# Kernel tuning notes

Measured on AMD Instinct MI355X. Metric: run time of the kernel, lower is better.

The kernel has to match this reference:

```python
import jax, jax.numpy as jnp
import numpy as np
import math

B, L, D, H = 2, 2048, 1024, 16
DH = D // H
TAU = 1.0
EPS_LN = 1e-12


def neural_sort(scores, tau=TAU):
    # scores: (B, n) -> soft permutation P_hat: (B, n, n)
    s = scores[..., None]                                   # (B,n,1)
    A = jnp.abs(s - jnp.swapaxes(s, 1, 2))                  # (B,n,n) pairwise |s_i - s_j|
    Bsum = jnp.sum(A, axis=-1, keepdims=True)               # row sums == A @ ones(n,n) columns
    n = scores.shape[-1]
    scaling = (n + 1 - 2 * (jnp.arange(n) + 1)).astype(scores.dtype)  # (n,)
    C = s * scaling[None, None, :]                          # (B,n,n)
    P_max = jnp.swapaxes(C - Bsum, 1, 2)
    return jax.nn.softmax(P_max / tau, axis=-1)


def euler_transform(v, delta, b_euler, log_scale, is_query):
    # v: (B,L,D); soft-sort channels, polar decompose, rotate, recompose
    Bv, Lv, Dv = v.shape
    scores = v.mean(axis=1)                                 # (B,D)
    P = neural_sort(scores)                                 # (B,D,D)
    v_sorted = jnp.einsum('bij,blj->bli', P, v)             # permute channel dim
    r, p = v_sorted[..., ::2], v_sorted[..., 1::2]          # (B,L,D/2)
    lam = jnp.sqrt(r * r + p * p + 1e-6)
    lam_d = jax.lax.stop_gradient(lam)
    theta = jnp.arctan2(p / lam_d, r / lam_d)
    theta = theta * delta
    if is_query:
        theta = theta + b_euler
    lam = lam * jnp.exp(jnp.clip(log_scale, -5.0, 5.0))
    out = jnp.stack([lam * jnp.cos(theta), lam * jnp.sin(theta)], axis=-1)
    return out.reshape(Bv, Lv, Dv)


def layer_norm(x, gamma, beta, eps=EPS_LN):
    mu = x.mean(axis=-1, keepdims=True)
    var = ((x - mu) ** 2).mean(axis=-1, keepdims=True)
    return (x - mu) / jnp.sqrt(var + eps) * gamma + beta


def forward(input_tensor, Wq, bq, Wk, bk, Wv, bv, Wd, bd, gamma, beta, delta, b_euler, log_scale):
    q = input_tensor @ Wq.T + bq
    k = input_tensor @ Wk.T + bk
    v = input_tensor @ Wv.T + bv
    q = euler_transform(q, delta, b_euler, log_scale, is_query=True)
    k = euler_transform(k, delta, b_euler, log_scale, is_query=False)
    def heads(x):
        return x.reshape(B, L, H, DH).transpose(0, 2, 1, 3)  # (B,H,L,DH)
    qh, kh, vh = heads(q), heads(k), heads(v)
    scores = jnp.einsum('bhqd,bhkd->bhqk', qh, kh) / math.sqrt(DH)
    probs = jax.nn.softmax(scores, axis=-1)                 # dropout off (eval)
    ctx = jnp.einsum('bhqk,bhkd->bhqd', probs, vh)
    ctx = ctx.transpose(0, 2, 1, 3).reshape(B, L, D)
    hidden = ctx @ Wd.T + bd
    return layer_norm(hidden + input_tensor, gamma, beta)


def setup_inputs() -> dict:
    key = jax.random.key(0)
    ks = jax.random.split(key, 16)
    s = 1.0 / math.sqrt(D)
    return {
        'input_tensor': jax.random.normal(ks[0], (B, L, D), jnp.float32),
        'Wq': jax.random.normal(ks[1], (D, D), jnp.float32) * s,
        'bq': jnp.zeros((D,), jnp.float32),
        'Wk': jax.random.normal(ks[2], (D, D), jnp.float32) * s,
        'bk': jnp.zeros((D,), jnp.float32),
        'Wv': jax.random.normal(ks[3], (D, D), jnp.float32) * s,
        'bv': jnp.zeros((D,), jnp.float32),
        'Wd': jax.random.normal(ks[4], (D, D), jnp.float32) * s,
        'bd': jnp.zeros((D,), jnp.float32),
        'gamma': jnp.ones((D,), jnp.float32),
        'beta': jnp.zeros((D,), jnp.float32),
        'delta': jnp.full((1, 1, D // 2), 0.1, jnp.float32),
        'b_euler': jnp.zeros((1, 1, D // 2), jnp.float32),
        'log_scale': jnp.zeros((1, 1, D // 2), jnp.float32),
    }


def reference(input_tensor, Wq, bq, Wk, bk, Wv, bv, Wd, bd, gamma, beta, delta, b_euler, log_scale):
    return forward(input_tensor, Wq, bq, Wk, bk, Wv, bv, Wd, bd, gamma, beta, delta, b_euler, log_scale)
```

## Files before the change

### kernel.cpp

```cpp
#include <hip/hip_runtime.h>


typedef unsigned short bf16_t;
typedef short frag_ab __attribute__((ext_vector_type(8)));
typedef float frag_cd __attribute__((ext_vector_type(4)));

#define BB 2
#define LL 2048
#define DD 1024
#define HH 16
#define DH 64

#define QSCALE 0.18033688f
#define EOFF  -17.3123404907f

__device__ __forceinline__ float b2f(bf16_t u) {
  union { unsigned int i; float f; } c; c.i = ((unsigned int)u) << 16; return c.f;
}
__device__ __forceinline__ bf16_t f2b(float f) {
  union { float f; unsigned int i; } c; c.f = f;
  unsigned int r = c.i + 0x7fffu + ((c.i >> 16) & 1u);
  return (bf16_t)(r >> 16);
}
__device__ __forceinline__ unsigned int fbits(float f) {
  union { float f; unsigned int i; } c; c.f = f; return c.i;
}
__device__ __forceinline__ float waveMax(float v) {
#pragma unroll
  for (int m = 32; m > 0; m >>= 1) v = fmaxf(v, __shfl_xor(v, m));
  return v;
}
__device__ __forceinline__ float waveSum(float v) {
#pragma unroll
  for (int m = 32; m > 0; m >>= 1) v += __shfl_xor(v, m);
  return v;
}

__device__ __forceinline__ void gll16(const bf16_t* g, bf16_t* l) {
  __builtin_amdgcn_global_load_lds(
      (const __attribute__((address_space(1))) void*)g,
      (__attribute__((address_space(3))) void*)l, 16, 0, 0);
}

__global__ __launch_bounds__(256) void prep_cast(const float* __restrict__ X,
                                                 const float* __restrict__ Wv,
                                                 const float* __restrict__ Wd,
                                                 bf16_t* __restrict__ Xb,
                                                 bf16_t* __restrict__ Wvb,
                                                 bf16_t* __restrict__ Wdb,
                                                 float* __restrict__ xmean) {
  const int bid = blockIdx.x;
  if (bid == 6144) {
    if (threadIdx.x < 256)
      for (int i = threadIdx.x; i < BB * DD; i += 256) xmean[i] = 0.f;
    return;
  }
  const float* in;
  bf16_t* out;
  int i;
  if (bid < 4096)      { in = X;  out = Xb;  i = bid * 256 + threadIdx.x; }
  else if (bid < 5120) { in = Wv; out = Wvb; i = (bid - 4096) * 256 + threadIdx.x; }
  else                 { in = Wd; out = Wdb; i = (bid - 5120) * 256 + threadIdx.x; }
  float4 v = ((const float4*)in)[i];
  ushort4 o;
  o.x = f2b(v.x); o.y = f2b(v.y); o.z = f2b(v.z); o.w = f2b(v.w);
  ((ushort4*)out)[i] = o;
}

__global__ __launch_bounds__(256) void cast_transpose_w(const float* __restrict__ Wq,
                                                        const float* __restrict__ Wk,
                                                        bf16_t* __restrict__ WqT,
                                                        bf16_t* __restrict__ WkT) {
  const float* W = blockIdx.z ? Wk : Wq;
  bf16_t* WT = blockIdx.z ? WkT : WqT;
  __shared__ bf16_t T[64][72];
  const int i0 = blockIdx.x * 64, m0 = blockIdx.y * 64;
  const int tid = threadIdx.x;
#pragma unroll
  for (int it = 0; it < 4; ++it) {
    const int idx = tid + it * 256;
    const int r = idx >> 4, c4 = (idx & 15) * 4;
    float4 v = *(const float4*)&W[(size_t)(i0 + r) * DD + m0 + c4];
    T[c4 + 0][r] = f2b(v.x);
    T[c4 + 1][r] = f2b(v.y);
    T[c4 + 2][r] = f2b(v.z);
    T[c4 + 3][r] = f2b(v.w);
  }
  __syncthreads();
#pragma unroll
  for (int it = 0; it < 2; ++it) {
    const int idx = tid + it * 256;
    const int r = idx >> 3, seg = idx & 7;
    *(uint4*)&WT[(size_t)(m0 + r) * DD + i0 + seg * 8] = *(const uint4*)&T[r][seg * 8];
  }
}

struct GemmB { const bf16_t* A; const bf16_t* Bm; const float* bias; float* Cf; bf16_t* Cb; };
struct GemmArgs { GemmB gb[6]; };

__global__ __launch_bounds__(256) void gemm128(GemmArgs ga, int M, int N, int K) {
  const GemmB g = ga.gb[blockIdx.z];
  const int bm = blockIdx.y * 128, bn = blockIdx.x * 128;
  __shared__ bf16_t As[128][32];
  __shared__ bf16_t Bs[128][32];
  bf16_t* As_f = &As[0][0];
  bf16_t* Bs_f = &Bs[0][0];
  const int tid = threadIdx.x;
  const int lane = tid & 63, w = tid >> 6;
  const int quad = lane >> 4, l16 = lane & 15;
  const int wm = (w >> 1) * 64, wn = (w & 1) * 64;
  const int wbase = w << 9;

  frag_cd acc[4][4];
#pragma unroll
  for (int i = 0; i < 4; ++i)
#pragma unroll
    for (int j = 0; j < 4; ++j)
#pragma unroll
      for (int r = 0; r < 4; ++r) acc[i][j][r] = 0.f;

  const int r0 = tid >> 2, s0 = (tid & 3) * 8;
  const int r1 = (tid + 256) >> 2, s1 = ((tid + 256) & 3) * 8;
  const size_t aoff0 = (size_t)(bm + r0) * K + s0;
  const size_t aoff1 = (size_t)(bm + r1) * K + s1;
  const size_t boff0 = (size_t)(bn + r0) * K + s0;
  const size_t boff1 = (size_t)(bn + r1) * K + s1;

  for (int k0 = 0; k0 < K; k0 += 32) {
    __syncthreads();
    gll16(g.A + aoff0 + k0, As_f + wbase);
    gll16(g.A + aoff1 + k0, As_f + 2048 + wbase);
    gll16(g.Bm + boff0 + k0, Bs_f + wbase);
    gll16(g.Bm + boff1 + k0, Bs_f + 2048 + wbase);
    __syncthreads();
    frag_ab af[4], bfr[4];
#pragma unroll
    for (int i = 0; i < 4; ++i) {
      af[i]  = *(const frag_ab*)&As[wm + i * 16 + l16][quad * 8];
      bfr[i] = *(const frag_ab*)&Bs[wn + i * 16 + l16][quad * 8];
    }
#pragma unroll
    for (int i = 0; i < 4; ++i)
#pragma unroll
      for (int j = 0; j < 4; ++j)
        acc[i][j] = __builtin_amdgcn_mfma_f32_16x16x32_bf16(af[i], bfr[j], acc[i][j], 0, 0, 0);
  }

#pragma unroll
  for (int i = 0; i < 4; ++i) {
#pragma unroll
    for (int r = 0; r < 4; ++r) {
      const int row = bm + wm + i * 16 + quad * 4 + r;
#pragma unroll
      for (int j = 0; j < 4; ++j) {
        const int col = bn + wn + j * 16 + l16;
        float v = acc[i][j][r];
        if (g.bias) v += g.bias[col];
        if (g.Cf) g.Cf[(size_t)row * N + col] = v;
        if (g.Cb) g.Cb[(size_t)row * N + col] = f2b(v);
      }
    }
  }
}

__global__ __launch_bounds__(256) void gemm64x64(GemmArgs ga, int M, int N, int K) {
  const GemmB g = ga.gb[blockIdx.z];
  const int bm = blockIdx.y * 64, bn = blockIdx.x * 64;
  __shared__ bf16_t As[64][32];
  __shared__ bf16_t Bs[64][32];
  bf16_t* As_f = &As[0][0];
  bf16_t* Bs_f = &Bs[0][0];
  const int tid = threadIdx.x;
  const int lane = tid & 63, w = tid >> 6;
  const int quad = lane >> 4, l16 = lane & 15;
  const int wm = (w >> 1) * 32, wn = (w & 1) * 32;
  const int wbase = w << 9;

  frag_cd acc[2][2];
#pragma unroll
  for (int i = 0; i < 2; ++i)
#pragma unroll
    for (int j = 0; j < 2; ++j)
#pragma unroll
      for (int r = 0; r < 4; ++r) acc[i][j][r] = 0.f;

  const int r0 = tid >> 2, s0 = (tid & 3) * 8;
  const size_t aoff0 = (size_t)(bm + r0) * K + s0;
  const size_t boff0 = (size_t)(bn + r0) * K + s0;

  for (int k0 = 0; k0 < K; k0 += 32) {
    __syncthreads();
    gll16(g.A + aoff0 + k0, As_f + wbase);
    gll16(g.Bm + boff0 + k0, Bs_f + wbase);
    __syncthreads();
    frag_ab af[2], bfr[2];
#pragma unroll
    for (int i = 0; i < 2; ++i) {
      af[i]  = *(const frag_ab*)&As[wm + i * 16 + l16][quad * 8];
      bfr[i] = *(const frag_ab*)&Bs[wn + i * 16 + l16][quad * 8];
    }
#pragma unroll
    for (int i = 0; i < 2; ++i)
#pragma unroll
      for (int j = 0; j < 2; ++j)
        acc[i][j] = __builtin_amdgcn_mfma_f32_16x16x32_bf16(af[i], bfr[j], acc[i][j], 0, 0, 0);
  }

#pragma unroll
  for (int i = 0; i < 2; ++i) {
#pragma unroll
    for (int r = 0; r < 4; ++r) {
      const int row = bm + wm + i * 16 + quad * 4 + r;
#pragma unroll
      for (int j = 0; j < 2; ++j) {
        const int col = bn + wn + j * 16 + l16;
        float v = acc[i][j][r];
        if (g.bias) v += g.bias[col];
        if (g.Cf) g.Cf[(size_t)row * N + col] = v;
        if (g.Cb) g.Cb[(size_t)row * N + col] = f2b(v);
      }
    }
  }
}

__global__ __launch_bounds__(256) void xmean_kernel(const float* __restrict__ X,
                                                    float* __restrict__ xmean) {
  const int d = blockIdx.x * 256 + threadIdx.x;
  const int b = blockIdx.z;
  const int l0 = blockIdx.y * 64;
  float s = 0.f;
  for (int l = l0; l < l0 + 64; ++l)
    s += X[((size_t)b * LL + l) * DD + d];
  atomicAdd(&xmean[b * DD + d], s * (1.f / (float)LL));
}

__global__ __launch_bounds__(256) void scores_gemm(const float* __restrict__ xmean,
                                                   const float* __restrict__ Wq,
                                                   const float* __restrict__ bq,
                                                   const float* __restrict__ Wk,
                                                   const float* __restrict__ bk,
                                                   float* __restrict__ scores) {
  const int w = threadIdx.x >> 6, lane = threadIdx.x & 63;
  const int idx = blockIdx.x * 4 + w;
  const int t = idx >> 11, b = (idx >> 10) & 1, i = idx & 1023;
  const float* W = t ? Wk : Wq;
  const float* bias = t ? bk : bq;
  const float* xm = xmean + b * DD;
  float sum = 0.f;
#pragma unroll
  for (int k = 0; k < 4; ++k) {
    float4 wv = *(const float4*)&W[(size_t)i * DD + k * 256 + lane * 4];
    float4 xv = *(const float4*)&xm[k * 256 + lane * 4];
    sum += wv.x * xv.x + wv.y * xv.y + wv.z * xv.z + wv.w * xv.w;
  }
  sum = waveSum(sum);
  if (lane == 0) scores[idx] = sum + bias[i];
}

__global__ __launch_bounds__(256) void bsum_kernel(const float* __restrict__ scores,
                                                   float* __restrict__ bsum) {
  __shared__ float sc[DD];
  const int z = blockIdx.x, jb = blockIdx.y, tid = threadIdx.x;
#pragma unroll
  for (int s = 0; s < 4; ++s) sc[tid + s * 256] = scores[z * DD + tid + s * 256];
  __syncthreads();
  const int j = jb * 256 + tid;
  const float si = sc[j];
  float s = 0.f;
  for (int m = 0; m < DD; m += 4) {
    float4 v = *(const float4*)&sc[m];
    s += fabsf(si - v.x) + fabsf(si - v.y) + fabsf(si - v.z) + fabsf(si - v.w);
  }
  bsum[z * DD + j] = s;
}

__global__ __launch_bounds__(256) void p_kernel(const float* __restrict__ scores,
                                                const float* __restrict__ bsum,
                                                const float* __restrict__ bq,
                                                const float* __restrict__ bk,
                                                bf16_t* __restrict__ Pq,
                                                bf16_t* __restrict__ Pk,
                                                float* __restrict__ bias4) {
  const int i = blockIdx.x;
  const int z = blockIdx.y;
  const int t = z >> 1, b = z & 1;
  const float* sc = scores + z * DD;
  const float* bs = bsum + z * DD;
  const float* bias = t ? bk : bq;
  const float scal = 1023.f - 2.f * (float)i;
  const int tid = threadIdx.x;
  __shared__ float redA[4], redB[4], redC[4];

  float lg[4], bb[4];
  float mx = -1e30f;
#pragma unroll
  for (int s = 0; s < 4; ++s) {
    const int j = tid + s * 256;
    lg[s] = sc[j] * scal - bs[j];
    bb[s] = bias[j];
    mx = fmaxf(mx, lg[s]);
  }
  mx = waveMax(mx);
  if ((tid & 63) == 0) redA[tid >> 6] = mx;
  __syncthreads();
  const float M = fmaxf(fmaxf(redA[0], redA[1]), fmaxf(redA[2], redA[3]));
  float sum = 0.f, dot = 0.f;
#pragma unroll
  for (int s = 0; s < 4; ++s) {
    lg[s] = __expf(lg[s] - M);
    sum += lg[s];
    dot += lg[s] * bb[s];
  }
  sum = waveSum(sum); dot = waveSum(dot);
  if ((tid & 63) == 0) { redB[tid >> 6] = sum; redC[tid >> 6] = dot; }
  __syncthreads();
  const float inv = 1.f / (redB[0] + redB[1] + redB[2] + redB[3]);
  bf16_t* P = (t ? Pk : Pq) + ((size_t)b << 20) + (size_t)i * DD;
#pragma unroll
  for (int s = 0; s < 4; ++s) P[tid + s * 256] = f2b(lg[s] * inv);
  if (tid == 0)
    bias4[t * 2048 + b * 1024 + i] = (redC[0] + redC[1] + redC[2] + redC[3]) * inv;
}

__global__ __launch_bounds__(256) void euler_transv(bf16_t* __restrict__ qs,
                                                    bf16_t* __restrict__ ks,
                                                    const float* __restrict__ delta,
                                                    const float* __restrict__ beul,
                                                    const float* __restrict__ lsc,
                                                    const bf16_t* __restrict__ vb,
                                                    bf16_t* __restrict__ vbT) {
  __shared__ bf16_t T[64][72];
  const int bid = blockIdx.x;
  const int tid = threadIdx.x;
  if (bid < 16384) {
    const int isq = (bid < 8192);
    unsigned int* buf = (unsigned int*)(isq ? qs : ks);
    const int idx = (isq ? bid : bid - 8192) * 256 + tid;
    const int c = idx & 511;
    const size_t n = idx >> 9;
    const unsigned int u = buf[n * 512 + c];
    const float r = b2f((bf16_t)(u & 0xffffu));
    const float p = b2f((bf16_t)(u >> 16));
    float lam = sqrtf(r * r + p * p + 1e-6f);
    float th = atan2f(p, r) * delta[c];
    if (isq) th += beul[c];
    lam *= __expf(fminf(fmaxf(lsc[c], -5.f), 5.f));
    if (isq) lam *= QSCALE;
    float sn, cs;
    __sincosf(th, &sn, &cs);
    buf[n * 512 + c] = ((unsigned int)f2b(lam * sn) << 16) | (unsigned int)f2b(lam * cs);
    return;
  }
  const int tb = bid - 16384;
  const int l0 = (tb & 31) * 64, d0 = ((tb >> 5) & 15) * 64, b = tb >> 9;
  for (int i = tid; i < 512; i += 256) {
    const int r = i >> 3, seg = i & 7;
    uint4 v = *(const uint4*)&vb[((size_t)b * LL + l0 + r) * DD + d0 + seg * 8];
    const bf16_t* vs = (const bf16_t*)&v;
#pragma unroll
    for (int j = 0; j < 8; ++j) T[seg * 8 + j][r] = vs[j];
  }
  __syncthreads();
  for (int i = tid; i < 512; i += 256) {
    const int r = i >> 3, seg = i & 7;
    *(uint4*)&vbT[((size_t)b * DD + d0 + r) * LL + l0 + seg * 8] =
        *(const uint4*)&T[r][seg * 8];
  }
}

__global__ __launch_bounds__(256) void attn_kernel(const bf16_t* __restrict__ Q,
                                                   const bf16_t* __restrict__ Kt,
                                                   const bf16_t* __restrict__ VT,
                                                   bf16_t* __restrict__ O) {
  const int bid = blockIdx.x;
  const int g = (bid & 7) + 8 * (bid >> 8);
  const int qt = (bid >> 3) & 31;
  const int b = g >> 4, h = g & 15;
  const int q0 = qt * 64;
  const int tid = threadIdx.x, w = tid >> 6, lane = tid & 63;
  const int quad = lane >> 4, l16 = lane & 15;
  __shared__ bf16_t Ks[64][72], Vs[80][72], Ps[64][72], Qs[64][72];
  const size_t base = ((size_t)b * LL) * DD + (size_t)h * DH;
  const size_t vtb = (size_t)(b * DD + h * DH) * LL;

  for (int i = tid; i < 16 * 72; i += 256) {
    const int r = i / 72;
    Vs[64 + r][i % 72] = (r == 0) ? (bf16_t)0x3F80 : (bf16_t)0;
  }
  for (int i = tid; i < 512; i += 256) {
    const int r = i >> 3, seg = i & 7;
    *(uint4*)&Qs[r][seg * 8] = *(const uint4*)&Q[base + (size_t)(q0 + r) * DD + seg * 8];
  }
  __syncthreads();
  frag_ab bq0 = *(const frag_ab*)&Qs[w * 16 + l16][quad * 8];
  frag_ab bq1 = *(const frag_ab*)&Qs[w * 16 + l16][32 + quad * 8];

  frag_cd o_[4], l5;
#pragma unroll
  for (int n = 0; n < 4; ++n)
#pragma unroll
    for (int r = 0; r < 4; ++r) o_[n][r] = 0.f;
#pragma unroll
  for (int r = 0; r < 4; ++r) l5[r] = 0.f;

  for (int kt = 0; kt < LL / 64; ++kt) {
    __syncthreads();
    for (int i = tid; i < 512; i += 256) {
      const int r = i >> 3, seg = i & 7;
      *(uint4*)&Ks[r][seg * 8] = *(const uint4*)&Kt[base + (size_t)(kt * 64 + r) * DD + seg * 8];
      *(uint4*)&Vs[r][seg * 8] = *(const uint4*)&VT[vtb + (size_t)r * LL + kt * 64 + seg * 8];
    }
    __syncthreads();

#pragma unroll
    for (int n = 0; n < 4; ++n) {
      frag_ab ak0 = *(const frag_ab*)&Ks[n * 16 + l16][quad * 8];
      frag_ab ak1 = *(const frag_ab*)&Ks[n * 16 + l16][32 + quad * 8];
      frag_cd z; z[0] = z[1] = z[2] = z[3] = EOFF;
      z = __builtin_amdgcn_mfma_f32_16x16x32_bf16(ak0, bq0, z, 0, 0, 0);
      z = __builtin_amdgcn_mfma_f32_16x16x32_bf16(ak1, bq1, z, 0, 0, 0);
      float p0 = __builtin_amdgcn_exp2f(z[0]);
      float p1 = __builtin_amdgcn_exp2f(z[1]);
      float p2 = __builtin_amdgcn_exp2f(z[2]);
      float p3 = __builtin_amdgcn_exp2f(z[3]);
      unsigned int u01 = __builtin_amdgcn_perm(fbits(p1), fbits(p0), 0x07060302u);
      unsigned int u23 = __builtin_amdgcn_perm(fbits(p3), fbits(p2), 0x07060302u);
      uint2 pk; pk.x = u01; pk.y = u23;
      *(uint2*)&Ps[w * 16 + l16][n * 16 + quad * 4] = pk;
    }

    frag_ab ap0 = *(const frag_ab*)&Ps[w * 16 + l16][quad * 8];
    frag_ab ap1 = *(const frag_ab*)&Ps[w * 16 + l16][32 + quad * 8];
#pragma unroll
    for (int n = 0; n < 4; ++n) {
      frag_ab bv0 = *(const frag_ab*)&Vs[n * 16 + l16][quad * 8];
      frag_ab bv1 = *(const frag_ab*)&Vs[n * 16 + l16][32 + quad * 8];
      o_[n] = __builtin_amdgcn_mfma_f32_16x16x32_bf16(ap0, bv0, o_[n], 0, 0, 0);
      o_[n] = __builtin_amdgcn_mfma_f32_16x16x32_bf16(ap1, bv1, o_[n], 0, 0, 0);
    }
    frag_ab bo0 = *(const frag_ab*)&Vs[64 + l16][quad * 8];
    frag_ab bo1 = *(const frag_ab*)&Vs[64 + l16][32 + quad * 8];
    l5 = __builtin_amdgcn_mfma_f32_16x16x32_bf16(ap0, bo0, l5, 0, 0, 0);
    l5 = __builtin_amdgcn_mfma_f32_16x16x32_bf16(ap1, bo1, l5, 0, 0, 0);
  }

  float lfin[4];
#pragma unroll
  for (int r = 0; r < 4; ++r) lfin[r] = 1.f / __shfl(l5[r], quad << 4);

#pragma unroll
  for (int n = 0; n < 4; ++n)
#pragma unroll
    for (int r = 0; r < 4; ++r) {
      const float v = o_[n][r] * lfin[r];
      O[base + (size_t)(q0 + w * 16 + quad * 4 + r) * DD + n * 16 + l16] = f2b(v);
    }
}

__global__ __launch_bounds__(256) void ln_kernel(const bf16_t* __restrict__ hidden,
                                                 const float* __restrict__ x0,
                                                 const float* __restrict__ gamma,
                                                 const float* __restrict__ beta,
                                                 float* __restrict__ out) {
  const int row = blockIdx.x;
  const int tid = threadIdx.x;
  __shared__ float red1[4], red2[4];
  float v[4];
  float s1 = 0.f, s2 = 0.f;
#pragma unroll
  for (int s = 0; s < 4; ++s) {
    const int c = tid + s * 256;
    const float x = b2f(hidden[(size_t)row * DD + c]) + x0[(size_t)row * DD + c];
    v[s] = x; s1 += x; s2 += x * x;
  }
  s1 = waveSum(s1); s2 = waveSum(s2);
  if ((tid & 63) == 0) { red1[tid >> 6] = s1; red2[tid >> 6] = s2; }
  __syncthreads();
  const float t1 = red1[0] + red1[1] + red1[2] + red1[3];
  const float t2 = red2[0] + red2[1] + red2[2] + red2[3];
  const float mu = t1 * (1.f / DD);
  const float var = t2 * (1.f / DD) - mu * mu;
  const float inv = rsqrtf(var + 1e-12f);
#pragma unroll
  for (int s = 0; s < 4; ++s) {
    const int c = tid + s * 256;
    out[(size_t)row * DD + c] = (v[s] - mu) * inv * gamma[c] + beta[c];
  }
}

extern "C" void kernel_launch(void* const* d_in, const int* in_sizes, int n_in,
                              void* d_out, int out_size, void* d_ws, size_t ws_size,
                              hipStream_t stream) {
  const float* X    = (const float*)d_in[0];
  const float* Wq   = (const float*)d_in[1];
  const float* bq   = (const float*)d_in[2];
  const float* Wk   = (const float*)d_in[3];
  const float* bk   = (const float*)d_in[4];
  const float* Wv   = (const float*)d_in[5];
  const float* bv   = (const float*)d_in[6];
  const float* Wd   = (const float*)d_in[7];
  const float* bd   = (const float*)d_in[8];
  const float* gam  = (const float*)d_in[9];
  const float* bet  = (const float*)d_in[10];
  const float* delt = (const float*)d_in[11];
  const float* beul = (const float*)d_in[12];
  const float* lsc  = (const float*)d_in[13];
  float* out = (float*)d_out;

  char* w = (char*)d_ws;
  const size_t MB = 1024ull * 1024ull;
  bf16_t* Xb  = (bf16_t*)(w + 0 * MB);
  bf16_t* Wvb = (bf16_t*)(w + 8 * MB);
  bf16_t* Wdb = (bf16_t*)(w + 10 * MB);
  bf16_t* WqT = (bf16_t*)(w + 12 * MB);
  bf16_t* WkT = (bf16_t*)(w + 14 * MB);
  bf16_t* Pq  = (bf16_t*)(w + 16 * MB);
  bf16_t* Pk  = (bf16_t*)(w + 20 * MB);
  bf16_t* Wp  = (bf16_t*)(w + 24 * MB);
  bf16_t* vb  = (bf16_t*)(w + 32 * MB);
  bf16_t* qs  = (bf16_t*)(w + 40 * MB);
  bf16_t* ks  = (bf16_t*)(w + 48 * MB);
  bf16_t* vbT = (bf16_t*)(w + 56 * MB);
  bf16_t* ctx = (bf16_t*)(w + 64 * MB);
  bf16_t* hid = (bf16_t*)(w + 24 * MB);
  float*  xmean  = (float*)(w + 72 * MB);
  float*  scores = (float*)(w + 72 * MB + 16384);
  float*  bsum   = (float*)(w + 72 * MB + 32768);
  float*  bias4  = (float*)(w + 72 * MB + 49152);

  const size_t WSZ = (size_t)DD * DD;

  prep_cast<<<dim3(6145), 256, 0, stream>>>(X, Wv, Wd, Xb, Wvb, Wdb, xmean);
  cast_transpose_w<<<dim3(16, 16, 2), 256, 0, stream>>>(Wq, Wk, WqT, WkT);

  xmean_kernel<<<dim3(4, 32, 2), 256, 0, stream>>>(X, xmean);
  scores_gemm<<<dim3(1024), 256, 0, stream>>>(xmean, Wq, bq, Wk, bk, scores);

  bsum_kernel<<<dim3(4, 4), 256, 0, stream>>>(scores, bsum);
  p_kernel<<<dim3(1024, 4), 256, 0, stream>>>(scores, bsum, bq, bk, Pq, Pk, bias4);

  GemmArgs gw = {};
  gw.gb[0] = {Pq,       WqT, nullptr, nullptr, Wp};
  gw.gb[1] = {Pq + WSZ, WqT, nullptr, nullptr, Wp + WSZ};
  gw.gb[2] = {Pk,       WkT, nullptr, nullptr, Wp + 2 * WSZ};
  gw.gb[3] = {Pk + WSZ, WkT, nullptr, nullptr, Wp + 3 * WSZ};
  gemm64x64<<<dim3(16, 16, 4), 256, 0, stream>>>(gw, DD, DD, DD);

  const size_t XHALF = (size_t)LL * DD;
  GemmArgs gs = {};
  gs.gb[0] = {Xb,         Wp,           bias4,        nullptr, qs};
  gs.gb[1] = {Xb + XHALF, Wp + WSZ,     bias4 + 1024, nullptr, qs + XHALF};
  gs.gb[2] = {Xb,         Wp + 2 * WSZ, bias4 + 2048, nullptr, ks};
  gs.gb[3] = {Xb + XHALF, Wp + 3 * WSZ, bias4 + 3072, nullptr, ks + XHALF};
  gs.gb[4] = {Xb,         Wvb,          bv,           nullptr, vb};
  gs.gb[5] = {Xb + XHALF, Wvb,          bv,           nullptr, vb + XHALF};
  gemm128<<<dim3(8, 16, 6), 256, 0, stream>>>(gs, LL, DD, DD);

  euler_transv<<<dim3(17408), 256, 0, stream>>>(qs, ks, delt, beul, lsc, vb, vbT);

  attn_kernel<<<dim3(1024), 256, 0, stream>>>(qs, ks, vbT, ctx);

  GemmArgs g4 = {};
  g4.gb[0] = {ctx, Wdb, bd, nullptr, hid};
  gemm64x64<<<dim3(16, 64, 1), 256, 0, stream>>>(g4, BB * LL, DD, DD);

  ln_kernel<<<dim3(BB * LL), 256, 0, stream>>>(hid, X, gam, bet, out);
}
```

Measured before the change: 310.7 us.

## Restructure attention kernel with double-buffered async LDS loads and swizzled tiles

Rewrites the attention kernel to use 128-thread blocks where each wave handles 32 query rows. K/V tiles are double-buffered and loaded with direct global-to-LDS loads under explicit vmcnt waits, so the next tile's load overlaps compute. LDS tiles use an XOR swizzle instead of padding to avoid bank conflicts. The row-sum is accumulated in registers from bf16-truncated probabilities instead of an extra MFMA against a ones column. It risks lower occupancy per block and correctness issues from the manual waitcnt and the truncation-consistent sums.

New measurement: 311.0 us. About the same (+0.1%).

```diff
diff --git a/kernel.cpp b/kernel.cpp
--- a/kernel.cpp
+++ b/kernel.cpp
@@ -25,6 +25,9 @@
 __device__ __forceinline__ unsigned int fbits(float f) {
   union { float f; unsigned int i; } c; c.f = f; return c.i;
 }
+__device__ __forceinline__ float tr16(float x) {
+  union { float f; unsigned int i; } c; c.f = x; c.i &= 0xffff0000u; return c.f;
+}
 __device__ __forceinline__ float waveMax(float v) {
 #pragma unroll
   for (int m = 32; m > 0; m >>= 1) v = fmaxf(v, __shfl_xor(v, m));
@@ -40,6 +43,10 @@
   __builtin_amdgcn_global_load_lds(
       (const __attribute__((address_space(1))) void*)g,
       (__attribute__((address_space(3))) void*)l, 16, 0, 0);
+}
+
+__device__ __forceinline__ frag_ab ld_tile(const bf16_t* base, int row, int chunk) {
+  return *(const frag_ab*)((const char*)base + (row << 7) + (((chunk ^ row) & 7) << 4));
 }
 
 __global__ __launch_bounds__(256) void prep_cast(const float* __restrict__ X,
@@ -368,93 +375,140 @@
   }
 }
 
-__global__ __launch_bounds__(256) void attn_kernel(const bf16_t* __restrict__ Q,
+__global__ __launch_bounds__(128) void attn_kernel(const bf16_t* __restrict__ Q,
                                                    const bf16_t* __restrict__ Kt,
                                                    const bf16_t* __restrict__ VT,
                                                    bf16_t* __restrict__ O) {
   const int bid = blockIdx.x;
-  const int g = (bid & 7) + 8 * (bid >> 8);
-  const int qt = (bid >> 3) & 31;
+  const int swz = (bid & 7) * 128 + (bid >> 3);
+  const int g = swz >> 5;
+  const int qt = swz & 31;
   const int b = g >> 4, h = g & 15;
   const int q0 = qt * 64;
   const int tid = threadIdx.x, w = tid >> 6, lane = tid & 63;
   const int quad = lane >> 4, l16 = lane & 15;
-  __shared__ bf16_t Ks[64][72], Vs[80][72], Ps[64][72], Qs[64][72];
-  const size_t base = ((size_t)b * LL) * DD + (size_t)h * DH;
+
+  __shared__ bf16_t Ks[2][64 * 64];
+  __shared__ bf16_t Vs[2][64 * 64];
+  __shared__ bf16_t Ps[64 * 64];
+
+  const size_t base = (size_t)b * LL * DD + (size_t)h * DH;
   const size_t vtb = (size_t)(b * DD + h * DH) * LL;
 
-  for (int i = tid; i < 16 * 72; i += 256) {
-    const int r = i / 72;
-    Vs[64 + r][i % 72] = (r == 0) ? (bf16_t)0x3F80 : (bf16_t)0;
-  }
-  for (int i = tid; i < 512; i += 256) {
-    const int r = i >> 3, seg = i & 7;
-    *(uint4*)&Qs[r][seg * 8] = *(const uint4*)&Q[base + (size_t)(q0 + r) * DD + seg * 8];
-  }
-  __syncthreads();
-  frag_ab bq0 = *(const frag_ab*)&Qs[w * 16 + l16][quad * 8];
-  frag_ab bq1 = *(const frag_ab*)&Qs[w * 16 + l16][32 + quad * 8];
-
-  frag_cd o_[4], l5;
-#pragma unroll
-  for (int n = 0; n < 4; ++n)
-#pragma unroll
-    for (int r = 0; r < 4; ++r) o_[n][r] = 0.f;
-#pragma unroll
-  for (int r = 0; r < 4; ++r) l5[r] = 0.f;
-
-  for (int kt = 0; kt < LL / 64; ++kt) {
-    __syncthreads();
-    for (int i = tid; i < 512; i += 256) {
-      const int r = i >> 3, seg = i & 7;
-      *(uint4*)&Ks[r][seg * 8] = *(const uint4*)&Kt[base + (size_t)(kt * 64 + r) * DD + seg * 8];
-      *(uint4*)&Vs[r][seg * 8] = *(const uint4*)&VT[vtb + (size_t)r * LL + kt * 64 + seg * 8];
-    }
-    __syncthreads();
-
+  frag_ab bq[2][2];
+#pragma unroll
+  for (int qg = 0; qg < 2; ++qg)
+#pragma unroll
+    for (int kh = 0; kh < 2; ++kh)
+      bq[qg][kh] = *(const frag_ab*)
+          &Q[base + (size_t)(q0 + w * 32 + qg * 16 + l16) * DD + kh * 32 + quad * 8];
+
+  frag_cd o_[2][4];
+#pragma unroll
+  for (int qg = 0; qg < 2; ++qg)
+#pragma unroll
+    for (int n = 0; n < 4; ++n)
+#pragma unroll
+      for (int r = 0; r < 4; ++r) o_[qg][n][r] = 0.f;
+  float ls0 = 0.f, ls1 = 0.f;
+
+  const int srow = lane >> 3;
+  const int cg = (lane & 7) ^ srow;
+  const int rbase = w * 32;
+
+  auto STAGE = [&](int buf, int kt) {
+#pragma unroll
+    for (int t = 0; t < 4; ++t) {
+      const int row = rbase + t * 8 + srow;
+      gll16(Kt + base + (size_t)(kt * 64 + row) * DD + cg * 8,
+            &Ks[buf][(rbase + t * 8) * 64]);
+      gll16(VT + vtb + (size_t)row * LL + kt * 64 + cg * 8,
+            &Vs[buf][(rbase + t * 8) * 64]);
+    }
+  };
+
+  STAGE(0, 0);
+  int cur = 0;
+  const int NT = LL / 64;
+  for (int kt = 0; kt < NT; ++kt) {
+    if (kt + 1 < NT) {
+      STAGE(cur ^ 1, kt + 1);
+      asm volatile("s_waitcnt vmcnt(8)" ::: "memory");
+    } else {
+      asm volatile("s_waitcnt vmcnt(0)" ::: "memory");
+    }
+    __builtin_amdgcn_s_barrier();
+
+    const bf16_t* Kb = Ks[cur];
+    const bf16_t* Vb = Vs[cur];
+
+    frag_ab ak[4][2];
 #pragma unroll
     for (int n = 0; n < 4; ++n) {
-      frag_ab ak0 = *(const frag_ab*)&Ks[n * 16 + l16][quad * 8];
-      frag_ab ak1 = *(const frag_ab*)&Ks[n * 16 + l16][32 + quad * 8];
-      frag_cd z; z[0] = z[1] = z[2] = z[3] = EOFF;
-      z = __builtin_amdgcn_mfma_f32_16x16x32_bf16(ak0, bq0, z, 0, 0, 0);
-      z = __builtin_amdgcn_mfma_f32_16x16x32_bf16(ak1, bq1, z, 0, 0, 0);
-      float p0 = __builtin_amdgcn_exp2f(z[0]);
-      float p1 = __builtin_amdgcn_exp2f(z[1]);
-      float p2 = __builtin_amdgcn_exp2f(z[2]);
-      float p3 = __builtin_amdgcn_exp2f(z[3]);
-      unsigned int u01 = __builtin_amdgcn_perm(fbits(p1), fbits(p0), 0x07060302u);
-      unsigned int u23 = __builtin_amdgcn_perm(fbits(p3), fbits(p2), 0x07060302u);
-      uint2 pk; pk.x = u01; pk.y = u23;
-      *(uint2*)&Ps[w * 16 + l16][n * 16 + quad * 4] = pk;
-    }
-
-    frag_ab ap0 = *(const frag_ab*)&Ps[w * 16 + l16][quad * 8];
-    frag_ab ap1 = *(const frag_ab*)&Ps[w * 16 + l16][32 + quad * 8];
+      ak[n][0] = ld_tile(Kb, n * 16 + l16, quad);
+      ak[n][1] = ld_tile(Kb, n * 16 + l16, 4 + quad);
+    }
+
+#pragma unroll
+    for (int qg = 0; qg < 2; ++qg) {
+      const int prow = rbase + qg * 16 + l16;
+      char* pb = (char*)Ps + prow * 128 + ((quad & 1) << 3);
+      float lacc = 0.f;
+#pragma unroll
+      for (int n = 0; n < 4; ++n) {
+        frag_cd z; z[0] = z[1] = z[2] = z[3] = EOFF;
+        z = __builtin_amdgcn_mfma_f32_16x16x32_bf16(ak[n][0], bq[qg][0], z, 0, 0, 0);
+        z = __builtin_amdgcn_mfma_f32_16x16x32_bf16(ak[n][1], bq[qg][1], z, 0, 0, 0);
+        float p0 = __builtin_amdgcn_exp2f(z[0]);
+        float p1 = __builtin_amdgcn_exp2f(z[1]);
+        float p2 = __builtin_amdgcn_exp2f(z[2]);
+        float p3 = __builtin_amdgcn_exp2f(z[3]);
+        lacc += (tr16(p0) + tr16(p1)) + (tr16(p2) + tr16(p3));
+        unsigned int u01 = __builtin_amdgcn_perm(fbits(p1), fbits(p0), 0x07060302u);
+        unsigned int u23 = __builtin_amdgcn_perm(fbits(p3), fbits(p2), 0x07060302u);
+        uint2 pk; pk.x = u01; pk.y = u23;
+        const int pc = 2 * n + (quad >> 1);
+        *(uint2*)(pb + (((pc ^ l16) & 7) << 4)) = pk;
+      }
+      if (qg == 0) ls0 += lacc; else ls1 += lacc;
+    }
+
+    frag_ab ap[2][2];
+#pragma unroll
+    for (int qg = 0; qg < 2; ++qg) {
+      const int prow = rbase + qg * 16 + l16;
+      ap[qg][0] = ld_tile(Ps, prow, quad);
+      ap[qg][1] = ld_tile(Ps, prow, 4 + quad);
+    }
 #pragma unroll
     for (int n = 0; n < 4; ++n) {
-      frag_ab bv0 = *(const frag_ab*)&Vs[n * 16 + l16][quad * 8];
-      frag_ab bv1 = *(const frag_ab*)&Vs[n * 16 + l16][32 + quad * 8];
-      o_[n] = __builtin_amdgcn_mfma_f32_16x16x32_bf16(ap0, bv0, o_[n], 0, 0, 0);
-      o_[n] = __builtin_amdgcn_mfma_f32_16x16x32_bf16(ap1, bv1, o_[n], 0, 0, 0);
-    }
-    frag_ab bo0 = *(const frag_ab*)&Vs[64 + l16][quad * 8];
-    frag_ab bo1 = *(const frag_ab*)&Vs[64 + l16][32 + quad * 8];
-    l5 = __builtin_amdgcn_mfma_f32_16x16x32_bf16(ap0, bo0, l5, 0, 0, 0);
-    l5 = __builtin_amdgcn_mfma_f32_16x16x32_bf16(ap1, bo1, l5, 0, 0, 0);
-  }
-
-  float lfin[4];
-#pragma unroll
-  for (int r = 0; r < 4; ++r) lfin[r] = 1.f / __shfl(l5[r], quad << 4);
-
-#pragma unroll
-  for (int n = 0; n < 4; ++n)
+      frag_ab bv0 = ld_tile(Vb, n * 16 + l16, quad);
+      frag_ab bv1 = ld_tile(Vb, n * 16 + l16, 4 + quad);
+#pragma unroll
+      for (int qg = 0; qg < 2; ++qg) {
+        o_[qg][n] = __builtin_amdgcn_mfma_f32_16x16x32_bf16(ap[qg][0], bv0, o_[qg][n], 0, 0, 0);
+        o_[qg][n] = __builtin_amdgcn_mfma_f32_16x16x32_bf16(ap[qg][1], bv1, o_[qg][n], 0, 0, 0);
+      }
+    }
+    __builtin_amdgcn_s_barrier();
+    cur ^= 1;
+  }
+
+#pragma unroll
+  for (int qg = 0; qg < 2; ++qg) {
+    float l = (qg == 0) ? ls0 : ls1;
+    l += __shfl_xor(l, 16);
+    l += __shfl_xor(l, 32);
 #pragma unroll
     for (int r = 0; r < 4; ++r) {
-      const float v = o_[n][r] * lfin[r];
-      O[base + (size_t)(q0 + w * 16 + quad * 4 + r) * DD + n * 16 + l16] = f2b(v);
-    }
+      const int src = (lane & 48) + ((lane & 48) >> 2) + r;
+      const float linv = 1.f / __shfl(l, src);
+      const int row = q0 + w * 32 + qg * 16 + quad * 4 + r;
+#pragma unroll
+      for (int n = 0; n < 4; ++n)
+        O[base + (size_t)row * DD + n * 16 + l16] = f2b(o_[qg][n][r] * linv);
+    }
+  }
 }
 
 __global__ __launch_bounds__(256) void ln_kernel(const bf16_t* __restrict__ hidden,
@@ -558,7 +612,7 @@
 
   euler_transv<<<dim3(17408), 256, 0, stream>>>(qs, ks, delt, beul, lsc, vb, vbT);
 
-  attn_kernel<<<dim3(1024), 256, 0, stream>>>(qs, ks, vbT, ctx);
+  attn_kernel<<<dim3(1024), 128, 0, stream>>>(qs, ks, vbT, ctx);
 
   GemmArgs g4 = {};
   g4.gb[0] = {ctx, Wdb, bd, nullptr, hid};
```
